# Performance work log

Hardware: AMD Instinct MI355X
Metric: run time of the kernel (lower is better)

The kernel has to match this reference:

```python
import jax, jax.numpy as jnp
import numpy as np

B, S, E = 2, 2048, 1024
H = 1344            # hidden_dim = ceil(1.3*1024/64)*64
NH = 4              # mLSTM heads
DH = H // NH        # 336
K = 4               # causal conv kernel size
NPH = H // 4        # headwise proj heads (qkv_proj_blocksize=4)
PD = H // NPH       # per-head proj dim = 4
EPS = 1e-6


def setup_inputs() -> dict:
    key = jax.random.key(0)
    ks = jax.random.split(key, 10)
    s_in = jnp.sqrt(2.0 / (5 * E))    # small_init(E)
    s_pd = jnp.sqrt(2.0 / (5 * PD))   # small_init per-head dim
    return {
        "x": jax.random.normal(ks[0], (B, S, E), jnp.float32),
        "W_up": jax.random.normal(ks[1], (E, 2 * H), jnp.float32) * s_in,
        "conv_k": jax.random.normal(ks[2], (K, 1, H), jnp.float32) * jnp.sqrt(2.0 / K),  # depthwise, WIO layout
        "conv_b": jnp.zeros((H,), jnp.float32),
        "Wq": jax.random.normal(ks[3], (NPH, PD, PD), jnp.float32) * s_pd,
        "Wk": jax.random.normal(ks[4], (NPH, PD, PD), jnp.float32) * s_pd,
        "Wv": jax.random.normal(ks[5], (NPH, PD, PD), jnp.float32) * s_pd,
        "W_ig": jax.random.normal(ks[6], (3 * H, NH), jnp.float32) * 0.01,
        "b_ig": jax.random.normal(ks[7], (NH,), jnp.float32) * 0.1,
        "W_fg": jax.random.normal(ks[8], (3 * H, NH), jnp.float32) * 0.01,
        "b_fg": jnp.linspace(3.0, 6.0, NH, dtype=jnp.float32),
        "ln_w": jnp.ones((H,), jnp.float32),
        "skip": jnp.ones((H,), jnp.float32),
        "W_down": jax.random.normal(ks[9], (H, E), jnp.float32) * (2.0 / 12 / np.sqrt(H)),
    }


def _headwise(x, W):
    # LinearHeadwiseExpand: block-diagonal projection over NPH heads of size PD
    xh = x.reshape(B, S, NPH, PD)
    return jnp.einsum('bshd,hdo->bsho', xh, W).reshape(B, S, H)


def _mlstm_cell(q, k, v, ig, fg):
    # parallel stabilized mLSTM; q,k,v: (B,NH,S,DH); ig,fg: (B,NH,S)
    logf = jax.nn.log_sigmoid(fg)
    c = jnp.cumsum(logf, axis=-1)                         # (B,NH,S)
    logfmat = c[..., :, None] - c[..., None, :]           # (B,NH,S,S) cumulative forget decay
    mask = jnp.tril(jnp.ones((S, S), bool))               # causal mask
    log_D = jnp.where(mask, logfmat, -jnp.inf) + ig[..., None, :]
    m = jnp.max(log_D, axis=-1, keepdims=True)            # rowwise stabilizer
    D = jnp.exp(log_D - m)
    qk = jnp.einsum('bnsd,bntd->bnst', q, k) * (DH ** -0.5)
    C = qk * D
    n = jnp.maximum(jnp.abs(jnp.sum(C, axis=-1, keepdims=True)), jnp.exp(-m))
    return jnp.einsum('bnst,bntd->bnsd', C / (n + EPS), v)


def reference(x, W_up, conv_k, conv_b, Wq, Wk, Wv, W_ig, b_ig, W_fg, b_fg, ln_w, skip, W_down):
    x_inner = x @ W_up                                    # (B,S,2H)
    x_m, z = jnp.split(x_inner, 2, axis=-1)
    # depthwise causal conv1d
    xp = jnp.pad(x_m, ((0, 0), (K - 1, 0), (0, 0)))
    xc = jax.lax.conv_general_dilated(
        xp, conv_k, (1,), 'VALID',
        dimension_numbers=('NWC', 'WIO', 'NWC'),
        feature_group_count=H) + conv_b
    act = jax.nn.silu(xc)
    q = _headwise(act, Wq)
    k = _headwise(act, Wk)
    v = _headwise(x_m, Wv)
    gin = jnp.concatenate([q, k, v], axis=-1)             # (B,S,3H)
    ig = jnp.transpose(gin @ W_ig + b_ig, (0, 2, 1))      # (B,NH,S)
    fg = jnp.transpose(gin @ W_fg + b_fg, (0, 2, 1))
    qh = jnp.transpose(q.reshape(B, S, NH, DH), (0, 2, 1, 3))
    kh = jnp.transpose(k.reshape(B, S, NH, DH), (0, 2, 1, 3))
    vh = jnp.transpose(v.reshape(B, S, NH, DH), (0, 2, 1, 3))
    h = _mlstm_cell(qh, kh, vh, ig, fg)                   # (B,NH,S,DH)
    # multi-head layernorm (per-head groupnorm over DH, scale only)
    mu = jnp.mean(h, axis=-1, keepdims=True)
    var = jnp.var(h, axis=-1, keepdims=True)
    hn = (h - mu) * jax.lax.rsqrt(var + 1e-5) * ln_w.reshape(NH, 1, DH)
    h_out = jnp.transpose(hn, (0, 2, 1, 3)).reshape(B, S, H)
    h_state = (h_out + skip * act) * jax.nn.silu(z)
    return h_state @ W_down
```

## Files before the change

kernel.cpp:

```cpp
#include <hip/hip_runtime.h>
#include <cmath>

#define DI __device__ __forceinline__

constexpr int B_=2, S_=2048, E_=1024, H_=1344, NH_=4, DH_=336;
constexpr int BS_=B_*S_, H2_=2*H_;
constexpr int NG_=B_*NH_*S_;

constexpr size_t N_X=(size_t)BS_*E_;
constexpr size_t N_WUP=(size_t)E_*H2_;
constexpr size_t N_WDN=(size_t)H_*E_;
constexpr size_t N_BSH=(size_t)BS_*H_;
constexpr size_t N_BSH2=(size_t)BS_*H2_;
constexpr size_t N_WH=5376, N_WG=16128, N_CK=4*H_;

constexpr size_t O_IGB = 64;
constexpr size_t O_LOGF= O_IGB + NG_;
constexpr size_t O_AB  = O_LOGF+ NG_;
constexpr size_t O_MB  = O_AB  + NG_;
constexpr size_t O_MTB = O_MB  + NG_;
constexpr size_t O_CK  = O_MTB + NG_;
constexpr size_t O_CB  = O_CK  + N_CK;
constexpr size_t O_WQ  = O_CB  + H_;
constexpr size_t O_WK  = O_WQ  + N_WH;
constexpr size_t O_WV  = O_WK  + N_WH;
constexpr size_t O_WIG = O_WV  + N_WH;
constexpr size_t O_BIG = O_WIG + N_WG;
constexpr size_t O_WFG = O_BIG + 16;
constexpr size_t O_BFG = O_WFG + N_WG;
constexpr size_t O_LNW = O_BFG + 16;
constexpr size_t O_SKP = O_LNW + H_;
constexpr size_t O_FX  = O_SKP + H_;
constexpr size_t O_FWUP= O_FX  + N_X;
constexpr size_t O_FWDN= O_FWUP+ N_WUP;
constexpr size_t O_XIN = O_FWDN+ N_WDN;
constexpr size_t O_ACT = O_XIN + N_BSH2;
constexpr size_t O_QB  = O_ACT + N_BSH;
constexpr size_t O_KB  = O_QB  + N_BSH;
constexpr size_t O_VB  = O_KB  + N_BSH;
constexpr size_t O_HOUT= O_VB  + N_BSH;

constexpr size_t KSPLIT_SHORTS=(size_t)8*128*11*64*8;
constexpr size_t VT_SHORTS=(size_t)8*64*22*64*8;

typedef __attribute__((ext_vector_type(8))) short bf16x8;
typedef __attribute__((ext_vector_type(4))) float f32x4;

DI float bf2f(unsigned int u){union{unsigned int i;float f;}v;v.i=(u&0xffffu)<<16;return v.f;}
DI unsigned short f2bf(float f){union{float f;unsigned int i;}v;v.f=f;unsigned int x=v.i;
  return (unsigned short)((x+0x7fffu+((x>>16)&1u))>>16);}
DI float siluf(float x){return x/(1.f+expf(-x));}
DI float logsigf(float x){return (x>=0.f)?-log1pf(expf(-x)):x-log1pf(expf(x));}
DI void load4(const float* p, float* d){float4 v=*reinterpret_cast<const float4*>(p);
  d[0]=v.x;d[1]=v.y;d[2]=v.z;d[3]=v.w;}

__global__ __launch_bounds__(256) void detect_k(const unsigned short* __restrict__ xraw,
                                                int* __restrict__ flag){
  __shared__ int cnt_s;
  if(threadIdx.x==0) cnt_s=0;
  __syncthreads();
  int c=0;
  for(int i=threadIdx.x;i<2048;i+=256){
    const unsigned e=(xraw[i]>>7)&0xFFu;
    if(e>=0x90u) c++;
  }
  atomicAdd(&cnt_s,c);
  __syncthreads();
  if(threadIdx.x==0) *flag=(cnt_s>16)?0:1;
}

constexpr int CV0=5376, CV1=CV0+1344, CV2=CV1+5376, CV3=CV2+5376, CV4=CV3+5376,
              CV5=CV4+16128, CV6=CV5+4, CV7=CV6+16128, CV8=CV7+4,
              CV9=CV8+1344, CVT=CV9+1344;
__global__ __launch_bounds__(256) void convall_k(
    const void* s0,const void* s1,const void* s2,const void* s3,const void* s4,
    const void* s5,const void* s6,const void* s7,const void* s8,const void* s9,
    const void* s10, float* __restrict__ ws, const int* __restrict__ flag){
  const int i=blockIdx.x*256+threadIdx.x;
  if(i>=CVT) return;
  const void* src; int off; size_t dst;
  if(i<CV0){src=s0; off=i;      dst=O_CK +off;}
  else if(i<CV1){src=s1; off=i-CV0; dst=O_CB +off;}
  else if(i<CV2){src=s2; off=i-CV1; dst=O_WQ +off;}
  else if(i<CV3){src=s3; off=i-CV2; dst=O_WK +off;}
  else if(i<CV4){src=s4; off=i-CV3; dst=O_WV +off;}
  else if(i<CV5){src=s5; off=i-CV4; dst=O_WIG+off;}
  else if(i<CV6){src=s6; off=i-CV5; dst=O_BIG+off;}
  else if(i<CV7){src=s7; off=i-CV6; dst=O_WFG+off;}
  else if(i<CV8){src=s8; off=i-CV7; dst=O_BFG+off;}
  else if(i<CV9){src=s9; off=i-CV8; dst=O_LNW+off;}
  else          {src=s10;off=i-CV9; dst=O_SKP+off;}
  ws[dst]=(*flag)?bf2f(((const unsigned short*)src)[off])
                 :((const float*)src)[off];
}

__global__ __launch_bounds__(256) void aprep_k(const void* __restrict__ src,
                                               const int* __restrict__ flag,
                                               int kcn,int ldk,int total,
                                               unsigned short* __restrict__ hi,
                                               unsigned short* __restrict__ lo){
  const int slot=blockIdx.x*256+threadIdx.x;
  if(slot>=total) return;
  const int l=slot&63, rest=slot>>6;
  const int kc=rest%kcn, mt=rest/kcn;
  const int row=mt*16+(l&15), k0=kc*32+(l>>4)*8;
  const int fl=flag?*flag:0;
  float v[8];
  if(fl){
    const unsigned short* s=(const unsigned short*)src+(size_t)row*ldk+k0;
    const uint4 u=*reinterpret_cast<const uint4*>(s);
    v[0]=bf2f(u.x);v[1]=bf2f(u.x>>16);v[2]=bf2f(u.y);v[3]=bf2f(u.y>>16);
    v[4]=bf2f(u.z);v[5]=bf2f(u.z>>16);v[6]=bf2f(u.w);v[7]=bf2f(u.w>>16);
  }else{
    const float* s=(const float*)src+(size_t)row*ldk+k0;
    load4(s,v); load4(s+4,v+4);
  }
  unsigned short h8[8], l8[8];
#pragma unroll
  for(int j=0;j<8;j++){ h8[j]=f2bf(v[j]); l8[j]=f2bf(v[j]-bf2f(h8[j])); }
  uint4 ph,pl;
  ph.x=(unsigned)h8[0]|((unsigned)h8[1]<<16); ph.y=(unsigned)h8[2]|((unsigned)h8[3]<<16);
  ph.z=(unsigned)h8[4]|((unsigned)h8[5]<<16); ph.w=(unsigned)h8[6]|((unsigned)h8[7]<<16);
  pl.x=(unsigned)l8[0]|((unsigned)l8[1]<<16); pl.y=(unsigned)l8[2]|((unsigned)l8[3]<<16);
  pl.z=(unsigned)l8[4]|((unsigned)l8[5]<<16); pl.w=(unsigned)l8[6]|((unsigned)l8[7]<<16);
  *reinterpret_cast<uint4*>(&hi[(size_t)slot*8])=ph;
  *reinterpret_cast<uint4*>(&lo[(size_t)slot*8])=pl;
}

__global__ __launch_bounds__(256) void bprep_k(const void* __restrict__ src,
                                               const int* __restrict__ flag,
                                               int kcn,int ldn,int total,
                                               unsigned short* __restrict__ hi,
                                               unsigned short* __restrict__ lo){
  const int slot=blockIdx.x*256+threadIdx.x;
  if(slot>=total) return;
  const int l=slot&63, rest=slot>>6;
  const int kc=rest%kcn, nt=rest/kcn;
  const int col=nt*16+(l&15), row0=kc*32+(l>>4)*8;
  const int fl=flag?*flag:0;
  float v[8];
  if(fl){
    const unsigned short* s=(const unsigned short*)src;
#pragma unroll
    for(int j=0;j<8;j++) v[j]=bf2f(s[(size_t)(row0+j)*ldn+col]);
  }else{
    const float* s=(const float*)src;
#pragma unroll
    for(int j=0;j<8;j++) v[j]=s[(size_t)(row0+j)*ldn+col];
  }
  unsigned short h8[8], l8[8];
#pragma unroll
  for(int j=0;j<8;j++){ h8[j]=f2bf(v[j]); l8[j]=f2bf(v[j]-bf2f(h8[j])); }
  uint4 ph,pl;
  ph.x=(unsigned)h8[0]|((unsigned)h8[1]<<16); ph.y=(unsigned)h8[2]|((unsigned)h8[3]<<16);
  ph.z=(unsigned)h8[4]|((unsigned)h8[5]<<16); ph.w=(unsigned)h8[6]|((unsigned)h8[7]<<16);
  pl.x=(unsigned)l8[0]|((unsigned)l8[1]<<16); pl.y=(unsigned)l8[2]|((unsigned)l8[3]<<16);
  pl.z=(unsigned)l8[4]|((unsigned)l8[5]<<16); pl.w=(unsigned)l8[6]|((unsigned)l8[7]<<16);
  *reinterpret_cast<uint4*>(&hi[(size_t)slot*8])=ph;
  *reinterpret_cast<uint4*>(&lo[(size_t)slot*8])=pl;
}

__global__ __launch_bounds__(256) void gemm3_k(
    const unsigned short* __restrict__ Ahi, const unsigned short* __restrict__ Alo,
    const unsigned short* __restrict__ Bhi, const unsigned short* __restrict__ Blo,
    void* __restrict__ C, const int* __restrict__ flag, int kcn, int ldc){
  const int t=threadIdx.x, w=t>>6, l=t&63, lm=l&15, quad=l>>4;
  const int bn=blockIdx.x*128, bm=blockIdx.y*128;
  const int mtg0=bm>>4, ntg0=bn>>4;

  __shared__ short TT[2][32*512];

  f32x4 acc[2][8];
#pragma unroll
  for(int g=0;g<2;g++)
#pragma unroll
    for(int nt=0;nt<8;nt++) acc[g][nt]={0.f,0.f,0.f,0.f};

  auto stage=[&](int buf,int kc){
#pragma unroll
    for(int j=0;j<8;j++){
      const int tr=w*8+j;
      const unsigned short* src;
      if(tr<8)       src=&Ahi[((size_t)(mtg0+tr   )*kcn+kc)*512+(size_t)l*8];
      else if(tr<16) src=&Alo[((size_t)(mtg0+tr-8 )*kcn+kc)*512+(size_t)l*8];
      else if(tr<24) src=&Bhi[((size_t)(ntg0+tr-16)*kcn+kc)*512+(size_t)l*8];
      else           src=&Blo[((size_t)(ntg0+tr-24)*kcn+kc)*512+(size_t)l*8];
      __builtin_amdgcn_global_load_lds(
        (const __attribute__((address_space(1))) unsigned int*)src,
        (__attribute__((address_space(3))) unsigned int*)&TT[buf][tr*512],
        16,0,0);
    }
  };

  auto compute=[&](int buf){
    const short* Tb=&TT[buf][0];
    const bf16x8 ah0=*reinterpret_cast<const bf16x8*>(&Tb[(2*w  )*512+l*8]);
    const bf16x8 ah1=*reinterpret_cast<const bf16x8*>(&Tb[(2*w+1)*512+l*8]);
    const bf16x8 al0=*reinterpret_cast<const bf16x8*>(&Tb[(8+2*w  )*512+l*8]);
    const bf16x8 al1=*reinterpret_cast<const bf16x8*>(&Tb[(8+2*w+1)*512+l*8]);
#pragma unroll
    for(int nt=0;nt<8;nt++){
      const bf16x8 bh=*reinterpret_cast<const bf16x8*>(&Tb[(16+nt)*512+l*8]);
      const bf16x8 bl=*reinterpret_cast<const bf16x8*>(&Tb[(24+nt)*512+l*8]);
      acc[0][nt]=__builtin_amdgcn_mfma_f32_16x16x32_bf16(ah0,bh,acc[0][nt],0,0,0);
      acc[0][nt]=__builtin_amdgcn_mfma_f32_16x16x32_bf16(al0,bh,acc[0][nt],0,0,0);
      acc[0][nt]=__builtin_amdgcn_mfma_f32_16x16x32_bf16(ah0,bl,acc[0][nt],0,0,0);
      acc[1][nt]=__builtin_amdgcn_mfma_f32_16x16x32_bf16(ah1,bh,acc[1][nt],0,0,0);
      acc[1][nt]=__builtin_amdgcn_mfma_f32_16x16x32_bf16(al1,bh,acc[1][nt],0,0,0);
      acc[1][nt]=__builtin_amdgcn_mfma_f32_16x16x32_bf16(ah1,bl,acc[1][nt],0,0,0);
    }
  };

  stage(0,0);
  for(int kc=0;kc<kcn;kc++){
    const int cur=kc&1;
    if(kc+1<kcn){
      stage(cur^1,kc+1);
      asm volatile("s_waitcnt vmcnt(8)" ::: "memory");
    } else {
      asm volatile("s_waitcnt vmcnt(0)" ::: "memory");
    }
    __builtin_amdgcn_s_barrier();
    compute(cur);
    __builtin_amdgcn_s_barrier();
  }

  const int bf=flag?*flag:0;
#pragma unroll
  for(int g=0;g<2;g++)
#pragma unroll
    for(int nt=0;nt<8;nt++)
#pragma unroll
      for(int r=0;r<4;r++){
        const size_t idx=(size_t)(bm+(2*w+g)*16+quad*4+r)*ldc+bn+nt*16+lm;
        if(bf) ((unsigned short*)C)[idx]=f2bf(acc[g][nt][r]);
        else   ((float*)C)[idx]=acc[g][nt][r];
      }
}

__global__ __launch_bounds__(256) void convqkv_k(const float* __restrict__ xin,
                                                 const float* __restrict__ ck,
                                                 const float* __restrict__ cb,
                                                 const float* __restrict__ Wq,
                                                 const float* __restrict__ Wk,
                                                 const float* __restrict__ Wv,
                                                 float* __restrict__ act,
                                                 float* __restrict__ qb,
                                                 float* __restrict__ kb,
                                                 float* __restrict__ vb){
  const int i=blockIdx.x*256+threadIdx.x;
  if(i>=BS_*(H_/4)) return;
  const int bs=i/(H_/4), ph=i-bs*(H_/4);
  const int b=bs>>11, s=bs&2047;
  const int base=ph*4;
  float xc[4];
#pragma unroll
  for(int d=0;d<4;d++) xc[d]=cb[base+d];
  float xm[4]={0.f,0.f,0.f,0.f};
#pragma unroll
  for(int w=0;w<4;w++){
    const int sr=s-3+w;
    if(sr>=0){
      float xv[4];
      load4(&xin[(size_t)(b*S_+sr)*H2_+base],xv);
#pragma unroll
      for(int d=0;d<4;d++) xc[d]+=xv[d]*ck[w*H_+base+d];
      if(w==3){ xm[0]=xv[0];xm[1]=xv[1];xm[2]=xv[2];xm[3]=xv[3]; }
    }
  }
  float a4[4];
#pragma unroll
  for(int d=0;d<4;d++) a4[d]=siluf(xc[d]);
  *reinterpret_cast<float4*>(&act[(size_t)bs*H_+base])
      =make_float4(a4[0],a4[1],a4[2],a4[3]);
  float q4[4],k4[4],v4[4];
#pragma unroll
  for(int o=0;o<4;o++){
    float q=0.f,k=0.f,v=0.f;
#pragma unroll
    for(int d=0;d<4;d++){
      q+=a4[d]*Wq[ph*16+d*4+o];
      k+=a4[d]*Wk[ph*16+d*4+o];
      v+=xm[d]*Wv[ph*16+d*4+o];
    }
    q4[o]=q;k4[o]=k;v4[o]=v;
  }
  const int nh=ph/84, dh0=(ph-nh*84)*4;
  const size_t off=((size_t)(b*NH_+nh)*S_+s)*DH_+dh0;
  *reinterpret_cast<float4*>(&qb[off])=make_float4(q4[0],q4[1],q4[2],q4[3]);
  *reinterpret_cast<float4*>(&kb[off])=make_float4(k4[0],k4[1],k4[2],k4[3]);
  *reinterpret_cast<float4*>(&vb[off])=make_float4(v4[0],v4[1],v4[2],v4[3]);
}

__global__ __launch_bounds__(256) void gates2_k(const float* __restrict__ qb,
                                                const float* __restrict__ kb,
                                                const float* __restrict__ vb,
                                                const float* __restrict__ Wig,
                                                const float* __restrict__ big,
                                                const float* __restrict__ Wfg,
                                                const float* __restrict__ bfg,
                                                float* __restrict__ igb,
                                                float* __restrict__ logfb){
  const int wid=(blockIdx.x*256+threadIdx.x)>>6;
  const int l=threadIdx.x&63;
  if(wid>=BS_) return;
  const int b=wid>>11, s=wid&2047;
  float aI0=0.f,aI1=0.f,aI2=0.f,aI3=0.f;
  float aF0=0.f,aF1=0.f,aF2=0.f,aF3=0.f;
  for(int nh=0;nh<NH_;nh++){
    const size_t rb=((size_t)(b*NH_+nh)*S_+s)*DH_;
    const int hb=nh*DH_;
    for(int dh=l;dh<DH_;dh+=64){
      const int h=hb+dh;
      const float q=qb[rb+dh], k=kb[rb+dh], v=vb[rb+dh];
      const float4 wiq=*reinterpret_cast<const float4*>(&Wig[(size_t)h*4]);
      const float4 wik=*reinterpret_cast<const float4*>(&Wig[(size_t)(H_+h)*4]);
      const float4 wiv=*reinterpret_cast<const float4*>(&Wig[(size_t)(2*H_+h)*4]);
      const float4 wfq=*reinterpret_cast<const float4*>(&Wfg[(size_t)h*4]);
      const float4 wfk=*reinterpret_cast<const float4*>(&Wfg[(size_t)(H_+h)*4]);
      const float4 wfv=*reinterpret_cast<const float4*>(&Wfg[(size_t)(2*H_+h)*4]);
      aI0+=q*wiq.x+k*wik.x+v*wiv.x;
      aI1+=q*wiq.y+k*wik.y+v*wiv.y;
      aI2+=q*wiq.z+k*wik.z+v*wiv.z;
      aI3+=q*wiq.w+k*wik.w+v*wiv.w;
      aF0+=q*wfq.x+k*wfk.x+v*wfv.x;
      aF1+=q*wfq.y+k*wfk.y+v*wfv.y;
      aF2+=q*wfq.z+k*wfk.z+v*wfv.z;
      aF3+=q*wfq.w+k*wfk.w+v*wfv.w;
    }
  }
#pragma unroll
  for(int m=1;m<64;m<<=1){
    aI0+=__shfl_xor(aI0,m); aI1+=__shfl_xor(aI1,m);
    aI2+=__shfl_xor(aI2,m); aI3+=__shfl_xor(aI3,m);
    aF0+=__shfl_xor(aF0,m); aF1+=__shfl_xor(aF1,m);
    aF2+=__shfl_xor(aF2,m); aF3+=__shfl_xor(aF3,m);
  }
  if(l==0){
    const size_t o0=(size_t)(b*NH_+0)*S_+s;
    const size_t o1=(size_t)(b*NH_+1)*S_+s;
    const size_t o2=(size_t)(b*NH_+2)*S_+s;
    const size_t o3=(size_t)(b*NH_+3)*S_+s;
    igb[o0]=aI0+big[0]; igb[o1]=aI1+big[1];
    igb[o2]=aI2+big[2]; igb[o3]=aI3+big[3];
    logfb[o0]=logsigf(aF0+bfg[0]); logfb[o1]=logsigf(aF1+bfg[1]);
    logfb[o2]=logsigf(aF2+bfg[2]); logfb[o3]=logsigf(aF3+bfg[3]);
  }
}

__global__ __launch_bounds__(256) void kprep_k(const float* __restrict__ kb,
                                               unsigned short* __restrict__ khi,
                                               unsigned short* __restrict__ klo){
  const int blk=blockIdx.x;
  const int head=blk>>7, tt=blk&127;
  const size_t obase=(size_t)blk*11*512;
  for(int slot=threadIdx.x; slot<704; slot+=256){
    const int dc=slot>>6, ll=slot&63, quad=ll>>4, lm=ll&15;
    const int tg=tt*16+lm, dbase=dc*32+quad*8;
    float v[8];
    if(dbase<336){
      load4(&kb[((size_t)head*S_+tg)*DH_+dbase],v);
      load4(&kb[((size_t)head*S_+tg)*DH_+dbase+4],v+4);
    } else { for(int j=0;j<8;j++) v[j]=0.f; }
    unsigned short hi8[8], lo8[8];
#pragma unroll
    for(int j=0;j<8;j++){
      hi8[j]=f2bf(v[j]);
      lo8[j]=f2bf(v[j]-bf2f(hi8[j]));
    }
    const size_t o=obase+(size_t)(dc*64+ll)*8;
    uint4 ph, pl;
    ph.x=(unsigned)hi8[0]|((unsigned)hi8[1]<<16); ph.y=(unsigned)hi8[2]|((unsigned)hi8[3]<<16);
    ph.z=(unsigned)hi8[4]|((unsigned)hi8[5]<<16); ph.w=(unsigned)hi8[6]|((unsigned)hi8[7]<<16);
    pl.x=(unsigned)lo8[0]|((unsigned)lo8[1]<<16); pl.y=(unsigned)lo8[2]|((unsigned)lo8[3]<<16);
    pl.z=(unsigned)lo8[4]|((unsigned)lo8[5]<<16); pl.w=(unsigned)lo8[6]|((unsigned)lo8[7]<<16);
    *reinterpret_cast<uint4*>(&khi[o])=ph;
    *reinterpret_cast<uint4*>(&klo[o])=pl;
  }
}

__global__ __launch_bounds__(256) void vprep_k(const float* vb,
                                               unsigned short* __restrict__ vTf,
                                               float* partz){
  const int blk=blockIdx.x;
  const int head=blk>>6, tc=blk&63;
  const size_t obase=(size_t)blk*22*512;
  for(int slot=threadIdx.x; slot<1408; slot+=256){
    const int ntg=slot>>6, ll=slot&63, quad=ll>>4, lm=ll&15;
    const int n=ntg*16+lm, t0=tc*32+quad*8;
    unsigned short h8[8];
#pragma unroll
    for(int j=0;j<8;j++){
      float val;
      if(n<336)       val=vb[((size_t)head*S_+t0+j)*DH_+n];
      else if(n==336) val=1.f;
      else            val=0.f;
      h8[j]=f2bf(val);
    }
    uint4 pk;
    pk.x=(unsigned)h8[0]|((unsigned)h8[1]<<16); pk.y=(unsigned)h8[2]|((unsigned)h8[3]<<16);
    pk.z=(unsigned)h8[4]|((unsigned)h8[5]<<16); pk.w=(unsigned)h8[6]|((unsigned)h8[7]<<16);
    *reinterpret_cast<uint4*>(&vTf[obase+(size_t)(ntg*64+ll)*8])=pk;
  }
  __syncthreads();
  const size_t zb=((size_t)head*2048+(size_t)tc*32)*336;
  for(int idx=threadIdx.x; idx<32*336; idx+=256) partz[zb+idx]=0.f;
}

__global__ __launch_bounds__(256) void scan_k(float* igm,
                                              const float* __restrict__ logfb,
                                              float* __restrict__ ab,float* __restrict__ Mb,
                                              float* __restrict__ mtb){
  const int head=blockIdx.x, t=threadIdx.x;
  __shared__ float sh[256];
  const float* lf=logfb+(size_t)head*S_;
  float* ig=igm+(size_t)head*S_;
  float lc[8];
  float run=0.f;
#pragma unroll
  for(int i=0;i<8;i++){ run+=lf[t*8+i]; lc[i]=run; }
  sh[t]=run;
  for(int st=1;st<256;st<<=1){
    __syncthreads();
    const float v=(t>=st)?sh[t-st]:0.f;
    __syncthreads();
    sh[t]+=v;
  }
  __syncthreads();
  const float off=(t==0)?0.f:sh[t-1];
  __syncthreads();
  float av[8],mv[8],cv[8];
  float mrun=-1e30f;
#pragma unroll
  for(int i=0;i<8;i++){
    cv[i]=off+lc[i];
    av[i]=ig[t*8+i]-cv[i];
    mrun=fmaxf(mrun,av[i]);
    mv[i]=mrun;
  }
  sh[t]=mrun;
  for(int st=1;st<256;st<<=1){
    __syncthreads();
    const float v=(t>=st)?sh[t-st]:-1e30f;
    __syncthreads();
    sh[t]=fmaxf(sh[t],v);
  }
  __syncthreads();
  const float moff=(t==0)?-1e30f:sh[t-1];
#pragma unroll
  for(int i=0;i<8;i++){
    const float Mi=fmaxf(moff,mv[i]);
    const size_t j=(size_t)head*S_+t*8+i;
    ab[j]=av[i]; Mb[j]=Mi; mtb[j]=cv[i]+Mi;
    ig[t*8+i]=0.f;
  }
}

__global__ __launch_bounds__(512,1) void mlstm8_k(
    const float* __restrict__ qb, const unsigned short* __restrict__ khi,
    const unsigned short* __restrict__ klo, const unsigned short* __restrict__ vTf,
    const float* __restrict__ ab, const float* __restrict__ Mb,
    float* __restrict__ part, float* __restrict__ rsum){
  const int bid=blockIdx.x;
  const int head=bid&7;
  const int rest=bid>>3;
  const int pairI=rest&7, seg=rest>>3;
  const int t=threadIdx.x, w=t>>6, l=t&63, lm=l&15, quad=l>>4;

  __shared__ short KV[2][66*512+128];
  __shared__ short Sc[8][16][40];

  const size_t hb=(size_t)head*S_;
  const float scale=0.05455447256f;

  const int sbA=pairI, sbB=15-pairI;
  const int nA=pairI+1, nTot=17;

  bf16x8 qh[11], ql[11];
  f32x4 accO[22];
  float Mr[4];
  int ws0=sbA*128+w*16;

  auto loadQ=[&](int ws0_){
    const float* qrow=qb+(hb+ws0_+lm)*DH_;
#pragma unroll
    for(int dc=0;dc<11;dc++){
      const int dbase=dc*32+quad*8;
      float v[8];
      if(dbase<336){ load4(qrow+dbase,v); load4(qrow+dbase+4,v+4); }
      else { for(int j=0;j<8;j++) v[j]=0.f; }
#pragma unroll
      for(int j=0;j<8;j++){
        const unsigned short h=f2bf(v[j]);
        qh[dc][j]=(short)h;
        ql[dc][j]=(short)f2bf(v[j]-bf2f(h));
      }
    }
#pragma unroll
    for(int r=0;r<4;r++) Mr[r]=Mb[hb+ws0_+quad*4+r];
#pragma unroll
    for(int n=0;n<22;n++) accO[n]={0.f,0.f,0.f,0.f};
  };

  auto itemC=[&](int i)->int{
    return (i<nA)? (seg+4*i) : (seg+4*(i-nA));
  };

  auto stage=[&](int buf,int c){
    const size_t kbase=(((size_t)head*128+(size_t)(2*c))*11)*512+(size_t)l*8;
    const size_t vbase=(((size_t)head*64+(size_t)c)*22)*512+(size_t)l*8;
#pragma unroll
    for(int j=0;j<9;j++){
      int tr=w+8*j;
      if(tr>=66) tr=w;
      const unsigned short* src;
      if(tr<22)      src=&khi[kbase+(size_t)tr*512];
      else if(tr<44) src=&klo[kbase+(size_t)(tr-22)*512];
      else           src=&vTf[vbase+(size_t)(tr-44)*512];
      __builtin_amdgcn_global_load_lds(
        (const __attribute__((address_space(1))) unsigned int*)src,
        (__attribute__((address_space(3))) unsigned int*)&KV[buf][(size_t)tr*512],
        16,0,0);
    }
    __builtin_amdgcn_global_load_lds(
      (const __attribute__((address_space(1))) unsigned int*)(ab+hb+(c<<5)+l),
      (__attribute__((address_space(3))) unsigned int*)&KV[buf][66*512],
      4,0,0);
  };

  auto compute=[&](int c,int buf){
    const int t0=c<<5;
    if(t0>ws0+15) return;
    const float* abl=reinterpret_cast<const float*>(&KV[buf][66*512]);
    const float al0=abl[lm];
    const float al1=abl[16+lm];
#pragma unroll
    for(int tt=0;tt<2;tt++){
      f32x4 a0={0,0,0,0}, a1={0,0,0,0}, a2={0,0,0,0};
#pragma unroll
      for(int dc=0;dc<11;dc++){
        const bf16x8 kh=*reinterpret_cast<const bf16x8*>(&KV[buf][(tt*11+dc)*512+l*8]);
        const bf16x8 kl=*reinterpret_cast<const bf16x8*>(&KV[buf][(22+tt*11+dc)*512+l*8]);
        a0=__builtin_amdgcn_mfma_f32_16x16x32_bf16(qh[dc],kh,a0,0,0,0);
        a1=__builtin_amdgcn_mfma_f32_16x16x32_bf16(ql[dc],kh,a1,0,0,0);
        a2=__builtin_amdgcn_mfma_f32_16x16x32_bf16(qh[dc],kl,a2,0,0,0);
      }
      const float al=(tt==0)?al0:al1;
      const int tg=t0+tt*16+lm;
#pragma unroll
      for(int r=0;r<4;r++){
        const int srow=quad*4+r;
        const float qk=a0[r]+a1[r]+a2[r];
        const float e=fminf(al-Mr[r],0.f);
        const float msk=(tg<=ws0+srow)?1.f:0.f;
        Sc[w][srow][tt*16+lm]=(short)f2bf(msk*(qk*scale*expf(e)));
      }
    }
    const bf16x8 scf=*reinterpret_cast<const bf16x8*>(&Sc[w][lm][quad*8]);
#pragma unroll
    for(int nt=0;nt<22;nt++){
      const bf16x8 vf=*reinterpret_cast<const bf16x8*>(&KV[buf][(44+nt)*512+l*8]);
      accO[nt]=__builtin_amdgcn_mfma_f32_16x16x32_bf16(scf,vf,accO[nt],0,0,0);
    }
  };

  auto epilogue=[&](){
    const size_t pbase=(size_t)head*2048+ws0;
#pragma unroll
    for(int nt=0;nt<22;nt++){
      const int col=nt*16+lm;
#pragma unroll
      for(int r=0;r<4;r++){
        const int srow=quad*4+r;
        const float val=accO[nt][r];
        if(col<336){ if(val!=0.f) atomicAdd(&part[(pbase+srow)*336+col],val); }
        else if(col==336){ if(val!=0.f) atomicAdd(&rsum[pbase+srow],val); }
      }
    }
  };

  loadQ(ws0);
  stage(0,itemC(0));
  int cur=0;
  for(int i=0;i<nTot;i++){
    if(i+1<nTot){
      stage(cur^1,itemC(i+1));
      asm volatile("s_waitcnt vmcnt(10)" ::: "memory");
    } else {
      asm volatile("s_waitcnt vmcnt(0)" ::: "memory");
    }
    __builtin_amdgcn_s_barrier();
    compute(itemC(i),cur);
    if(i==nA-1){
      epilogue();
      ws0=sbB*128+w*16;
      loadQ(ws0);
    }
    __builtin_amdgcn_s_barrier();
    cur^=1;
  }
  epilogue();
}

__global__ __launch_bounds__(256) void finalize2_k(const float* __restrict__ part,
                                                   const float* __restrict__ rsum,
                                                   const float* __restrict__ mtb,
                                                   const float* __restrict__ lnw,
                                                   const float* __restrict__ skip,
                                                   const float* __restrict__ act,
                                                   const float* __restrict__ xin,
                                                   float* __restrict__ hs){
  const int sblk=blockIdx.x, head=blockIdx.y;
  const int bI=head>>2, nh=head&3;
  const int s0=sblk*32;
  const int t=threadIdx.x, row=t>>3, sub=t&7;
  __shared__ float red1[32][8], red2[32][8];
  __shared__ float mu_s[32], rs_s[32], inv_s[32];
  const size_t pbase=(size_t)head*2048+s0;
  const float* prow=part+(pbase+row)*336;
  float s1=0.f,s2=0.f;
  for(int c=sub;c<336;c+=8){ const float v=prow[c]; s1+=v; s2+=v*v; }
  red1[row][sub]=s1; red2[row][sub]=s2;
  __syncthreads();
  if(sub==0){
    float a1=0.f,a2=0.f;
#pragma unroll
    for(int j=0;j<8;j++){ a1+=red1[row][j]; a2+=red2[row][j]; }
    const float mt=mtb[(size_t)head*S_+s0+row];
    const float nn=fmaxf(fabsf(rsum[pbase+row]), expf(fminf(fmaxf(-mt,-60.f),60.f)));
    const float inv=1.f/(nn+1e-6f);
    const float mu=a1*inv/336.f;
    const float var=a2*inv*inv/336.f-mu*mu;
    inv_s[row]=inv; mu_s[row]=mu;
    rs_s[row]=rsqrtf(fmaxf(var,0.f)+1e-5f);
  }
  __syncthreads();
  const float inv=inv_s[row], mu=mu_s[row], rs=rs_s[row];
  const size_t bsrow=(size_t)(bI*S_+s0+row);
  float* orow=hs+bsrow*H_+nh*DH_;
  const float* arow=act+bsrow*H_+nh*DH_;
  const float* zrow=xin+bsrow*H2_+H_+nh*DH_;
  const float* srw=skip+nh*DH_;
  const float* lrw=lnw+nh*DH_;
  for(int c=sub;c<336;c+=8){
    const float hn=(prow[c]*inv-mu)*rs*lrw[c];
    orow[c]=(hn+srw[c]*arow[c])*siluf(zrow[c]);
  }
}

extern "C" void kernel_launch(void* const* d_in, const int* in_sizes, int n_in,
                              void* d_out, int out_size, void* d_ws, size_t ws_size,
                              hipStream_t stream){
  float* ws=(float*)d_ws;
  int* flag=(int*)ws;

  float* igb  = ws+O_IGB;
  float* logfb= ws+O_LOGF;
  float* ab   = ws+O_AB;
  float* Mbuf = ws+O_MB;
  float* mtb  = ws+O_MTB;
  float* f_ck = ws+O_CK;
  float* f_cb = ws+O_CB;
  float* f_wq = ws+O_WQ;
  float* f_wk = ws+O_WK;
  float* f_wv = ws+O_WV;
  float* f_wig= ws+O_WIG;
  float* f_big= ws+O_BIG;
  float* f_wfg= ws+O_WFG;
  float* f_bfg= ws+O_BFG;
  float* f_lnw= ws+O_LNW;
  float* f_skp= ws+O_SKP;
  float* xin  = ws+O_XIN;
  float* act  = ws+O_ACT;
  float* qb   = ws+O_QB;
  float* kb   = ws+O_KB;
  float* vb   = ws+O_VB;

  unsigned short* xhi  =(unsigned short*)(ws+O_FX);   unsigned short* xlo  =xhi+N_X;
  unsigned short* wuphi=(unsigned short*)(ws+O_FWUP); unsigned short* wuplo=wuphi+N_WUP;
  unsigned short* wdnhi=(unsigned short*)(ws+O_FWDN); unsigned short* wdnlo=wdnhi+N_WDN;
  unsigned short* khi=(unsigned short*)(ws+O_FX);
  unsigned short* klo=khi+KSPLIT_SHORTS;
  unsigned short* vTf=(unsigned short*)kb;
  unsigned short* hshi=(unsigned short*)kb;
  unsigned short* hslo=hshi+N_BSH;
  float* partb=vb;
  float* rsumb=igb;
  float* hs   = qb;

  detect_k<<<1,256,0,stream>>>((const unsigned short*)d_in[0],flag);
  convall_k<<<(CVT+255)/256,256,0,stream>>>(d_in[2],d_in[3],d_in[4],d_in[5],d_in[6],
                                            d_in[7],d_in[8],d_in[9],d_in[10],d_in[11],
                                            d_in[12],ws,flag);

  aprep_k<<<(256*32*64+255)/256,256,0,stream>>>(d_in[0],flag,32,1024,256*32*64,xhi,xlo);
  bprep_k<<<(168*32*64+255)/256,256,0,stream>>>(d_in[1],flag,32,2688,168*32*64,wuphi,wuplo);
  gemm3_k<<<dim3(2688/128,4096/128),256,0,stream>>>(xhi,xlo,wuphi,wuplo,xin,nullptr,32,H2_);

  convqkv_k<<<(BS_*(H_/4)+255)/256,256,0,stream>>>(xin,f_ck,f_cb,f_wq,f_wk,f_wv,
                                                   act,qb,kb,vb);
  gates2_k<<<(BS_*64+255)/256,256,0,stream>>>(qb,kb,vb,f_wig,f_big,f_wfg,f_bfg,igb,logfb);
  kprep_k<<<8*128,256,0,stream>>>(kb,khi,klo);
  vprep_k<<<8*64,256,0,stream>>>(vb,vTf,partb);
  bprep_k<<<(64*42*64+255)/256,256,0,stream>>>(d_in[13],flag,42,1024,64*42*64,wdnhi,wdnlo);
  scan_k<<<B_*NH_,256,0,stream>>>(igb,logfb,ab,Mbuf,mtb);
  mlstm8_k<<<256,512,0,stream>>>(qb,khi,klo,vTf,ab,Mbuf,partb,rsumb);
  finalize2_k<<<dim3(S_/32,B_*NH_),256,0,stream>>>(partb,rsumb,mtb,f_lnw,f_skp,act,xin,hs);
  aprep_k<<<(256*42*64+255)/256,256,0,stream>>>(hs,nullptr,42,1344,256*42*64,hshi,hslo);
  gemm3_k<<<dim3(1024/128,4096/128),256,0,stream>>>(hshi,hslo,wdnhi,wdnlo,d_out,flag,42,E_);
}
```

Measured before the change: 470.0 us.

## Fuse K/V prep kernels, fold bf16 split into finalize, simplify mLSTM staging

Merges kprep and vprep into a single launch, and has finalize write the hi/lo bf16 tiled layout straight into the down-projection operand buffers, which removes the separate aprep pass and the fp32 hs round trip. The mLSTM kernel drops the LDS-staged decay vector and reads ab from global memory. Its fine-grained vmcnt waits are replaced by __syncthreads, which may reduce overlap of the next tile's loads with compute. vTf moves to a separate workspace region so it no longer aliases kb, which the hshi/hslo outputs now occupy.

```diff
diff --git a/kernel.cpp b/kernel.cpp
--- a/kernel.cpp
+++ b/kernel.cpp
@@ -348,63 +348,64 @@
   }
 }
 
-__global__ __launch_bounds__(256) void kprep_k(const float* __restrict__ kb,
-                                               unsigned short* __restrict__ khi,
-                                               unsigned short* __restrict__ klo){
+__global__ __launch_bounds__(256) void kvprep_k(const float* __restrict__ kb,
+                                                const float* vb,
+                                                unsigned short* __restrict__ khi,
+                                                unsigned short* __restrict__ klo,
+                                                unsigned short* __restrict__ vTf,
+                                                float* partz){
   const int blk=blockIdx.x;
-  const int head=blk>>7, tt=blk&127;
-  const size_t obase=(size_t)blk*11*512;
-  for(int slot=threadIdx.x; slot<704; slot+=256){
-    const int dc=slot>>6, ll=slot&63, quad=ll>>4, lm=ll&15;
-    const int tg=tt*16+lm, dbase=dc*32+quad*8;
-    float v[8];
-    if(dbase<336){
-      load4(&kb[((size_t)head*S_+tg)*DH_+dbase],v);
-      load4(&kb[((size_t)head*S_+tg)*DH_+dbase+4],v+4);
-    } else { for(int j=0;j<8;j++) v[j]=0.f; }
-    unsigned short hi8[8], lo8[8];
-#pragma unroll
-    for(int j=0;j<8;j++){
-      hi8[j]=f2bf(v[j]);
-      lo8[j]=f2bf(v[j]-bf2f(hi8[j]));
-    }
-    const size_t o=obase+(size_t)(dc*64+ll)*8;
-    uint4 ph, pl;
-    ph.x=(unsigned)hi8[0]|((unsigned)hi8[1]<<16); ph.y=(unsigned)hi8[2]|((unsigned)hi8[3]<<16);
-    ph.z=(unsigned)hi8[4]|((unsigned)hi8[5]<<16); ph.w=(unsigned)hi8[6]|((unsigned)hi8[7]<<16);
-    pl.x=(unsigned)lo8[0]|((unsigned)lo8[1]<<16); pl.y=(unsigned)lo8[2]|((unsigned)lo8[3]<<16);
-    pl.z=(unsigned)lo8[4]|((unsigned)lo8[5]<<16); pl.w=(unsigned)lo8[6]|((unsigned)lo8[7]<<16);
-    *reinterpret_cast<uint4*>(&khi[o])=ph;
-    *reinterpret_cast<uint4*>(&klo[o])=pl;
-  }
-}
-
-__global__ __launch_bounds__(256) void vprep_k(const float* vb,
-                                               unsigned short* __restrict__ vTf,
-                                               float* partz){
-  const int blk=blockIdx.x;
-  const int head=blk>>6, tc=blk&63;
-  const size_t obase=(size_t)blk*22*512;
-  for(int slot=threadIdx.x; slot<1408; slot+=256){
-    const int ntg=slot>>6, ll=slot&63, quad=ll>>4, lm=ll&15;
-    const int n=ntg*16+lm, t0=tc*32+quad*8;
-    unsigned short h8[8];
-#pragma unroll
-    for(int j=0;j<8;j++){
-      float val;
-      if(n<336)       val=vb[((size_t)head*S_+t0+j)*DH_+n];
-      else if(n==336) val=1.f;
-      else            val=0.f;
-      h8[j]=f2bf(val);
-    }
-    uint4 pk;
-    pk.x=(unsigned)h8[0]|((unsigned)h8[1]<<16); pk.y=(unsigned)h8[2]|((unsigned)h8[3]<<16);
-    pk.z=(unsigned)h8[4]|((unsigned)h8[5]<<16); pk.w=(unsigned)h8[6]|((unsigned)h8[7]<<16);
-    *reinterpret_cast<uint4*>(&vTf[obase+(size_t)(ntg*64+ll)*8])=pk;
-  }
-  __syncthreads();
-  const size_t zb=((size_t)head*2048+(size_t)tc*32)*336;
-  for(int idx=threadIdx.x; idx<32*336; idx+=256) partz[zb+idx]=0.f;
+  if(blk<1024){
+    const int head=blk>>7, tt=blk&127;
+    const size_t obase=(size_t)blk*11*512;
+    for(int slot=threadIdx.x; slot<704; slot+=256){
+      const int dc=slot>>6, ll=slot&63, quad=ll>>4, lm=ll&15;
+      const int tg=tt*16+lm, dbase=dc*32+quad*8;
+      float v[8];
+      if(dbase<336){
+        load4(&kb[((size_t)head*S_+tg)*DH_+dbase],v);
+        load4(&kb[((size_t)head*S_+tg)*DH_+dbase+4],v+4);
+      } else { for(int j=0;j<8;j++) v[j]=0.f; }
+      unsigned short hi8[8], lo8[8];
+#pragma unroll
+      for(int j=0;j<8;j++){
+        hi8[j]=f2bf(v[j]);
+        lo8[j]=f2bf(v[j]-bf2f(hi8[j]));
+      }
+      const size_t o=obase+(size_t)(dc*64+ll)*8;
+      uint4 ph, pl;
+      ph.x=(unsigned)hi8[0]|((unsigned)hi8[1]<<16); ph.y=(unsigned)hi8[2]|((unsigned)hi8[3]<<16);
+      ph.z=(unsigned)hi8[4]|((unsigned)hi8[5]<<16); ph.w=(unsigned)hi8[6]|((unsigned)hi8[7]<<16);
+      pl.x=(unsigned)lo8[0]|((unsigned)lo8[1]<<16); pl.y=(unsigned)lo8[2]|((unsigned)lo8[3]<<16);
+      pl.z=(unsigned)lo8[4]|((unsigned)lo8[5]<<16); pl.w=(unsigned)lo8[6]|((unsigned)lo8[7]<<16);
+      *reinterpret_cast<uint4*>(&khi[o])=ph;
+      *reinterpret_cast<uint4*>(&klo[o])=pl;
+    }
+  } else {
+    const int vblk=blk-1024;
+    const int head=vblk>>6, tc=vblk&63;
+    const size_t obase=(size_t)vblk*22*512;
+    for(int slot=threadIdx.x; slot<1408; slot+=256){
+      const int ntg=slot>>6, ll=slot&63, quad=ll>>4, lm=ll&15;
+      const int n=ntg*16+lm, t0=tc*32+quad*8;
+      unsigned short h8[8];
+#pragma unroll
+      for(int j=0;j<8;j++){
+        float val;
+        if(n<336)       val=vb[((size_t)head*S_+t0+j)*DH_+n];
+        else if(n==336) val=1.f;
+        else            val=0.f;
+        h8[j]=f2bf(val);
+      }
+      uint4 pk;
+      pk.x=(unsigned)h8[0]|((unsigned)h8[1]<<16); pk.y=(unsigned)h8[2]|((unsigned)h8[3]<<16);
+      pk.z=(unsigned)h8[4]|((unsigned)h8[5]<<16); pk.w=(unsigned)h8[6]|((unsigned)h8[7]<<16);
+      *reinterpret_cast<uint4*>(&vTf[obase+(size_t)(ntg*64+ll)*8])=pk;
+    }
+    __syncthreads();
+    const size_t zb=((size_t)head*2048+(size_t)tc*32)*336;
+    for(int idx=threadIdx.x; idx<32*336; idx+=256) partz[zb+idx]=0.f;
+  }
 }
 
 __global__ __launch_bounds__(256) void scan_k(float* igm,
@@ -456,7 +457,7 @@
   }
 }
 
-__global__ __launch_bounds__(512,1) void mlstm8_k(
+__global__ __launch_bounds__(512,1) void mlstm6_k(
     const float* __restrict__ qb, const unsigned short* __restrict__ khi,
     const unsigned short* __restrict__ klo, const unsigned short* __restrict__ vTf,
     const float* __restrict__ ab, const float* __restrict__ Mb,
@@ -467,7 +468,7 @@
   const int pairI=rest&7, seg=rest>>3;
   const int t=threadIdx.x, w=t>>6, l=t&63, lm=l&15, quad=l>>4;
 
-  __shared__ short KV[2][66*512+128];
+  __shared__ short KV[2][66*512];
   __shared__ short Sc[8][16][40];
 
   const size_t hb=(size_t)head*S_;
@@ -511,29 +512,25 @@
     const size_t vbase=(((size_t)head*64+(size_t)c)*22)*512+(size_t)l*8;
 #pragma unroll
     for(int j=0;j<9;j++){
-      int tr=w+8*j;
-      if(tr>=66) tr=w;
-      const unsigned short* src;
-      if(tr<22)      src=&khi[kbase+(size_t)tr*512];
-      else if(tr<44) src=&klo[kbase+(size_t)(tr-22)*512];
-      else           src=&vTf[vbase+(size_t)(tr-44)*512];
-      __builtin_amdgcn_global_load_lds(
-        (const __attribute__((address_space(1))) unsigned int*)src,
-        (__attribute__((address_space(3))) unsigned int*)&KV[buf][(size_t)tr*512],
-        16,0,0);
-    }
-    __builtin_amdgcn_global_load_lds(
-      (const __attribute__((address_space(1))) unsigned int*)(ab+hb+(c<<5)+l),
-      (__attribute__((address_space(3))) unsigned int*)&KV[buf][66*512],
-      4,0,0);
+      const int tr=w+8*j;
+      if(tr<66){
+        const unsigned short* src;
+        if(tr<22)      src=&khi[kbase+(size_t)tr*512];
+        else if(tr<44) src=&klo[kbase+(size_t)(tr-22)*512];
+        else           src=&vTf[vbase+(size_t)(tr-44)*512];
+        __builtin_amdgcn_global_load_lds(
+          (const __attribute__((address_space(1))) unsigned int*)src,
+          (__attribute__((address_space(3))) unsigned int*)&KV[buf][(size_t)tr*512],
+          16,0,0);
+      }
+    }
   };
 
   auto compute=[&](int c,int buf){
     const int t0=c<<5;
     if(t0>ws0+15) return;
-    const float* abl=reinterpret_cast<const float*>(&KV[buf][66*512]);
-    const float al0=abl[lm];
-    const float al1=abl[16+lm];
+    const float al0=ab[hb+t0+lm];
+    const float al1=ab[hb+t0+16+lm];
 #pragma unroll
     for(int tt=0;tt<2;tt++){
       f32x4 a0={0,0,0,0}, a1={0,0,0,0}, a2={0,0,0,0};
@@ -581,35 +578,31 @@
 
   loadQ(ws0);
   stage(0,itemC(0));
+  __syncthreads();
   int cur=0;
   for(int i=0;i<nTot;i++){
-    if(i+1<nTot){
-      stage(cur^1,itemC(i+1));
-      asm volatile("s_waitcnt vmcnt(10)" ::: "memory");
-    } else {
-      asm volatile("s_waitcnt vmcnt(0)" ::: "memory");
-    }
-    __builtin_amdgcn_s_barrier();
+    if(i+1<nTot) stage(cur^1,itemC(i+1));
     compute(itemC(i),cur);
     if(i==nA-1){
       epilogue();
       ws0=sbB*128+w*16;
       loadQ(ws0);
     }
-    __builtin_amdgcn_s_barrier();
+    __syncthreads();
     cur^=1;
   }
   epilogue();
 }
 
-__global__ __launch_bounds__(256) void finalize2_k(const float* __restrict__ part,
+__global__ __launch_bounds__(256) void finalize3_k(const float* __restrict__ part,
                                                    const float* __restrict__ rsum,
                                                    const float* __restrict__ mtb,
                                                    const float* __restrict__ lnw,
                                                    const float* __restrict__ skip,
                                                    const float* __restrict__ act,
                                                    const float* __restrict__ xin,
-                                                   float* __restrict__ hs){
+                                                   unsigned short* __restrict__ hshi,
+                                                   unsigned short* __restrict__ hslo){
   const int sblk=blockIdx.x, head=blockIdx.y;
   const int bI=head>>2, nh=head&3;
   const int s0=sblk*32;
@@ -636,15 +629,22 @@
   }
   __syncthreads();
   const float inv=inv_s[row], mu=mu_s[row], rs=rs_s[row];
-  const size_t bsrow=(size_t)(bI*S_+s0+row);
-  float* orow=hs+bsrow*H_+nh*DH_;
-  const float* arow=act+bsrow*H_+nh*DH_;
-  const float* zrow=xin+bsrow*H2_+H_+nh*DH_;
+  const size_t gbs=(size_t)(bI*S_+s0+row);
+  const float* arow=act+gbs*H_+nh*DH_;
+  const float* zrow=xin+gbs*H2_+H_+nh*DH_;
   const float* srw=skip+nh*DH_;
   const float* lrw=lnw+nh*DH_;
+  const size_t mtbase=(gbs>>4)*42;
+  const int lbase=(int)(gbs&15);
   for(int c=sub;c<336;c+=8){
     const float hn=(prow[c]*inv-mu)*rs*lrw[c];
-    orow[c]=(hn+srw[c]*arow[c])*siluf(zrow[c]);
+    const float val=(hn+srw[c]*arow[c])*siluf(zrow[c]);
+    const int h=nh*DH_+c;
+    const int kc=h>>5, quad=(h>>3)&3, j=h&7;
+    const size_t slot=(mtbase+kc)*64+lbase+16*quad;
+    const unsigned short hi=f2bf(val);
+    hshi[slot*8+j]=hi;
+    hslo[slot*8+j]=f2bf(val-bf2f(hi));
   }
 }
 
@@ -681,12 +681,11 @@
   unsigned short* wdnhi=(unsigned short*)(ws+O_FWDN); unsigned short* wdnlo=wdnhi+N_WDN;
   unsigned short* khi=(unsigned short*)(ws+O_FX);
   unsigned short* klo=khi+KSPLIT_SHORTS;
-  unsigned short* vTf=(unsigned short*)kb;
+  unsigned short* vTf=(unsigned short*)(ws+O_HOUT);
   unsigned short* hshi=(unsigned short*)kb;
   unsigned short* hslo=hshi+N_BSH;
   float* partb=vb;
   float* rsumb=igb;
-  float* hs   = qb;
 
   detect_k<<<1,256,0,stream>>>((const unsigned short*)d_in[0],flag);
   convall_k<<<(CVT+255)/256,256,0,stream>>>(d_in[2],d_in[3],d_in[4],d_in[5],d_in[6],
@@ -700,12 +699,11 @@
   convqkv_k<<<(BS_*(H_/4)+255)/256,256,0,stream>>>(xin,f_ck,f_cb,f_wq,f_wk,f_wv,
                                                    act,qb,kb,vb);
   gates2_k<<<(BS_*64+255)/256,256,0,stream>>>(qb,kb,vb,f_wig,f_big,f_wfg,f_bfg,igb,logfb);
-  kprep_k<<<8*128,256,0,stream>>>(kb,khi,klo);
-  vprep_k<<<8*64,256,0,stream>>>(vb,vTf,partb);
+  kvprep_k<<<1024+512,256,0,stream>>>(kb,vb,khi,klo,vTf,partb);
   bprep_k<<<(64*42*64+255)/256,256,0,stream>>>(d_in[13],flag,42,1024,64*42*64,wdnhi,wdnlo);
   scan_k<<<B_*NH_,256,0,stream>>>(igb,logfb,ab,Mbuf,mtb);
-  mlstm8_k<<<256,512,0,stream>>>(qb,khi,klo,vTf,ab,Mbuf,partb,rsumb);
-  finalize2_k<<<dim3(S_/32,B_*NH_),256,0,stream>>>(partb,rsumb,mtb,f_lnw,f_skp,act,xin,hs);
-  aprep_k<<<(256*42*64+255)/256,256,0,stream>>>(hs,nullptr,42,1344,256*42*64,hshi,hslo);
+  mlstm6_k<<<256,512,0,stream>>>(qb,khi,klo,vTf,ab,Mbuf,partb,rsumb);
+  finalize3_k<<<dim3(S_/32,B_*NH_),256,0,stream>>>(partb,rsumb,mtb,f_lnw,f_skp,act,xin,
+                                                   hshi,hslo);
   gemm3_k<<<dim3(1024/128,4096/128),256,0,stream>>>(hshi,hslo,wdnhi,wdnlo,d_out,flag,42,E_);
 }
```

New measurement: 461.4 us. Within noise of the previous version (-1.8%).
